# Performance work log

Measured on AMD Instinct MI355X. Metric: run time of the kernel, lower is better.

Reference implementation:

```python
import jax, jax.numpy as jnp
import numpy as np

B, S, D = 4, 1024, 1024
H = 16
DK = D // H  # 64
F = 4096
EPS = 1e-6


def layer_norm(x, gamma, beta):
    mu = jnp.mean(x, axis=-1, keepdims=True)
    var = jnp.mean(jnp.square(x - mu), axis=-1, keepdims=True)
    return (x - mu) * jax.lax.rsqrt(var + EPS) * gamma + beta


def setup_inputs() -> dict:
    key = jax.random.key(0)
    ks = jax.random.split(key, 16)
    sd = 0.02
    return {
        "x": jax.random.normal(ks[0], (B, S, D), dtype=jnp.float32),
        "Wq": jax.random.normal(ks[1], (H, D, DK), dtype=jnp.float32) * sd,
        "bq": jnp.zeros((H, DK), dtype=jnp.float32),
        "Wk": jax.random.normal(ks[2], (H, D, DK), dtype=jnp.float32) * sd,
        "bk": jnp.zeros((H, DK), dtype=jnp.float32),
        "Wv": jax.random.normal(ks[3], (H, D, DK), dtype=jnp.float32) * sd,
        "bv": jnp.zeros((H, DK), dtype=jnp.float32),
        "Wo": jax.random.normal(ks[4], (D, D), dtype=jnp.float32) * sd,
        "bo": jnp.zeros((D,), dtype=jnp.float32),
        "W1": jax.random.normal(ks[5], (D, F), dtype=jnp.float32) * sd,
        "b1": jnp.zeros((F,), dtype=jnp.float32),
        "W2": jax.random.normal(ks[6], (F, D), dtype=jnp.float32) * sd,
        "b2": jnp.zeros((D,), dtype=jnp.float32),
        "g1": jnp.ones((D,), dtype=jnp.float32),
        "be1": jnp.zeros((D,), dtype=jnp.float32),
        "g2": jnp.ones((D,), dtype=jnp.float32),
        "be2": jnp.zeros((D,), dtype=jnp.float32),
    }


def reference(x, Wq, bq, Wk, bk, Wv, bv, Wo, bo, W1, b1, W2, b2, g1, be1, g2, be2):
    # Per-head Dense projections, expressed as one batched einsum.
    # q/k/v: [B, H, S, DK]
    q = jnp.einsum('bsd,hdk->bhsk', x, Wq) + bq[:, None, :]
    k = jnp.einsum('bsd,hdk->bhsk', x, Wk) + bk[:, None, :]
    v = jnp.einsum('bsd,hdk->bhsk', x, Wv) + bv[:, None, :]
    scale = 1.0 / jnp.sqrt(jnp.float32(DK))
    scores = jnp.einsum('bhqk,bhsk->bhqs', q, k) * scale  # [B,H,S,S]
    attn = jax.nn.softmax(scores, axis=-1)
    ctx = jnp.einsum('bhqs,bhsk->bhqk', attn, v)  # [B,H,S,DK]
    # concat heads along last dim -> [B,S,D]
    ctx = jnp.transpose(ctx, (0, 2, 1, 3)).reshape(B, S, D)
    mh = ctx @ Wo + bo
    # dropout is identity at inference
    h1 = layer_norm(mh + x, g1, be1)
    ffn = jax.nn.relu(h1 @ W1 + b1) @ W2 + b2
    out = layer_norm(h1 + ffn, g2, be2)
    return out
```

## Files before the change

kernel.cpp:

```cpp
#include <hip/hip_runtime.h>
#include <hip/hip_bf16.h>
#include <stdint.h>


typedef __bf16 bf16x8 __attribute__((ext_vector_type(8)));
typedef float f32x4 __attribute__((ext_vector_type(4)));

__device__ __forceinline__ f32x4 mfma16(bf16x8 a, bf16x8 b, f32x4 c) {
  return __builtin_amdgcn_mfma_f32_16x16x32_bf16(a, b, c, 0, 0, 0);
}

__device__ __forceinline__ void gload_lds16(const void* g, void* l) {
  typedef const unsigned int __attribute__((address_space(1)))* GP;
  typedef unsigned int __attribute__((address_space(3)))* LP;
  __builtin_amdgcn_global_load_lds((GP)(uintptr_t)g,
                                   (LP)(unsigned int)(uintptr_t)l, 16, 0, 0);
}

template <int EPI>
__global__ __launch_bounds__(256, 2) void gemm_bt(
    const __bf16* __restrict__ A, const __bf16* __restrict__ BT,
    const float* __restrict__ bias, float* __restrict__ Cf,
    __bf16* __restrict__ Cb, int M, int N, int K)
{
  __shared__ __attribute__((aligned(16))) __bf16 As[128 * 32];
  __shared__ __attribute__((aligned(16))) __bf16 Bs[128 * 32];
  const int tid = threadIdx.x;
  const int lane = tid & 63;
  const int w = tid >> 6;
  const int wr = w >> 1, wc = w & 1;
  const int l15 = lane & 15, lhi = lane >> 4;
  const int m0 = blockIdx.y * 128, n0 = blockIdx.x * 128;

  const f32x4 fz = {0.f, 0.f, 0.f, 0.f};
  f32x4 acc[4][4];
#pragma unroll
  for (int i = 0; i < 4; i++)
#pragma unroll
    for (int j = 0; j < 4; j++) acc[i][j] = fz;

  const int arow = tid >> 2;
  const int acol = (tid & 3) * 8;
  const __bf16* Ag = A + (long)(m0 + arow) * K + acol;
  const __bf16* Bg = BT + (long)(n0 + arow) * K + acol;
  __bf16* Al = &As[tid * 8];
  __bf16* Bl = &Bs[tid * 8];

  for (int k0 = 0; k0 < K; k0 += 32) {
    gload_lds16(Ag + k0, Al);
    gload_lds16(Ag + k0 + 64 * (long)K, Al + 2048);
    gload_lds16(Bg + k0, Bl);
    gload_lds16(Bg + k0 + 64 * (long)K, Bl + 2048);
    __syncthreads();
    bf16x8 a[4], b[4];
#pragma unroll
    for (int i = 0; i < 4; i++) {
      a[i] = *(const bf16x8*)&As[(wr * 64 + i * 16 + l15) * 32 + lhi * 8];
      b[i] = *(const bf16x8*)&Bs[(wc * 64 + i * 16 + l15) * 32 + lhi * 8];
    }
#pragma unroll
    for (int i = 0; i < 4; i++)
#pragma unroll
      for (int j = 0; j < 4; j++) acc[i][j] = mfma16(a[i], b[j], acc[i][j]);
    __syncthreads();
  }

  if (EPI == 0) {
#pragma unroll
    for (int i = 0; i < 4; i++) {
      const int mB = m0 + wr * 64 + i * 16 + lhi * 4;
#pragma unroll
      for (int j = 0; j < 4; j++) {
        const int n = n0 + wc * 64 + j * 16 + l15;
        const float bs = bias[n];
#pragma unroll
        for (int r = 0; r < 4; r++)
          Cf[(long)(mB + r) * N + n] = acc[i][j][r] + bs;
      }
    }
  } else if (EPI == 1) {
#pragma unroll
    for (int i = 0; i < 4; i++) {
      const int mB = m0 + wr * 64 + i * 16 + lhi * 4;
#pragma unroll
      for (int j = 0; j < 4; j++) {
        const int n = n0 + wc * 64 + j * 16 + l15;
        const float bs = bias[n];
#pragma unroll
        for (int r = 0; r < 4; r++) {
          float v = acc[i][j][r] + bs;
          v = v > 0.f ? v : 0.f;
          Cb[(long)(mB + r) * N + n] = (__bf16)v;
        }
      }
    }
  } else {
#pragma unroll
    for (int i = 0; i < 4; i++) {
      const int mB = m0 + wr * 64 + i * 16 + lhi * 4;
#pragma unroll
      for (int j = 0; j < 4; j++) {
        const int n = n0 + wc * 64 + j * 16 + l15;
        const int proj = n >> 10, h = (n >> 6) & 15, dk = n & 63;
        const float bs = bias[n];
#pragma unroll
        for (int r = 0; r < 4; r++) {
          const int m = mB + r;
          const int b = m >> 10, sidx = m & 1023;
          Cb[(long)proj * 4194304 +
             ((long)(b * 16 + h) * 1024 + sidx) * 64 + dk] =
              (__bf16)(acc[i][j][r] + bs);
        }
      }
    }
  }
}

__global__ __launch_bounds__(256, 2) void attn_kernel(
    const __bf16* __restrict__ qg_, const __bf16* __restrict__ kg_,
    const __bf16* __restrict__ vg_, __bf16* __restrict__ ctx)
{
  __shared__ __attribute__((aligned(16))) __bf16 Ks[64 * 64];
  __shared__ __attribute__((aligned(16))) __bf16 Vt[64 * 64];
  __shared__ __attribute__((aligned(16))) __bf16 Ps[4][16 * 64];
  const int tid = threadIdx.x, lane = tid & 63, w = tid >> 6;
  const int l15 = lane & 15, lhi = lane >> 4;
  const int bh = blockIdx.y;
  const int b = bh >> 4, h = bh & 15;
  const int q0 = blockIdx.x * 64 + w * 16;

  const __bf16* qg = qg_ + ((long)bh * 1024 + q0) * 64;
  const __bf16* kg = kg_ + (long)bh * 1024 * 64;
  const __bf16* vg = vg_ + (long)bh * 1024 * 64;

  bf16x8 qa[2];
  qa[0] = *(const bf16x8*)&qg[l15 * 64 + lhi * 8];
  qa[1] = *(const bf16x8*)&qg[l15 * 64 + 32 + lhi * 8];

  const f32x4 fz = {0.f, 0.f, 0.f, 0.f};
  float mrun[4], lrun[4];
  f32x4 o[4];
#pragma unroll
  for (int r = 0; r < 4; r++) { mrun[r] = -1e30f; lrun[r] = 0.f; }
#pragma unroll
  for (int n = 0; n < 4; n++) o[n] = fz;

  const int lr = tid >> 2;
  const int lc = (tid & 3) * 16;

  for (int t = 0; t < 16; ++t) {
    __syncthreads();
    {
      const __bf16* krow = kg + (long)(t * 64 + lr) * 64 + lc;
      *(int4*)&Ks[lr * 64 + lc] = *(const int4*)krow;
      *(int4*)&Ks[lr * 64 + lc + 8] = *(const int4*)(krow + 8);
      const __bf16* vrow = vg + (long)(t * 64 + lr) * 64 + lc;
      int4 v0 = *(const int4*)vrow;
      int4 v1 = *(const int4*)(vrow + 8);
      const __bf16* e0 = (const __bf16*)&v0;
      const __bf16* e1 = (const __bf16*)&v1;
#pragma unroll
      for (int j = 0; j < 8; j++) Vt[(lc + j) * 64 + lr] = e0[j];
#pragma unroll
      for (int j = 0; j < 8; j++) Vt[(lc + 8 + j) * 64 + lr] = e1[j];
    }
    __syncthreads();

    f32x4 s[4];
#pragma unroll
    for (int n = 0; n < 4; n++) s[n] = fz;
#pragma unroll
    for (int kk = 0; kk < 2; kk++)
#pragma unroll
      for (int n = 0; n < 4; n++) {
        bf16x8 kb =
            *(const bf16x8*)&Ks[(n * 16 + l15) * 64 + kk * 32 + lhi * 8];
        s[n] = mfma16(qa[kk], kb, s[n]);
      }

    float alpha[4];
    float p[4][4];
#pragma unroll
    for (int r = 0; r < 4; r++) {
      float mx = -1e30f;
#pragma unroll
      for (int n = 0; n < 4; n++) {
        s[n][r] *= 0.125f;
        mx = fmaxf(mx, s[n][r]);
      }
#pragma unroll
      for (int off = 8; off; off >>= 1) mx = fmaxf(mx, __shfl_xor(mx, off));
      const float mnew = fmaxf(mrun[r], mx);
      alpha[r] = __expf(mrun[r] - mnew);
      float ps = 0.f;
#pragma unroll
      for (int n = 0; n < 4; n++) {
        const float pv = __expf(s[n][r] - mnew);
        p[n][r] = pv;
        ps += pv;
      }
#pragma unroll
      for (int off = 8; off; off >>= 1) ps += __shfl_xor(ps, off);
      mrun[r] = mnew;
      lrun[r] = lrun[r] * alpha[r] + ps;
    }
#pragma unroll
    for (int n = 0; n < 4; n++)
#pragma unroll
      for (int r = 0; r < 4; r++) o[n][r] *= alpha[r];

#pragma unroll
    for (int n = 0; n < 4; n++)
#pragma unroll
      for (int r = 0; r < 4; r++)
        Ps[w][(lhi * 4 + r) * 64 + n * 16 + l15] = (__bf16)p[n][r];
    asm volatile("s_waitcnt lgkmcnt(0)" ::: "memory");

#pragma unroll
    for (int kk = 0; kk < 2; kk++) {
      bf16x8 pa = *(const bf16x8*)&Ps[w][l15 * 64 + kk * 32 + lhi * 8];
#pragma unroll
      for (int n = 0; n < 4; n++) {
        bf16x8 vb =
            *(const bf16x8*)&Vt[(n * 16 + l15) * 64 + kk * 32 + lhi * 8];
        o[n] = mfma16(pa, vb, o[n]);
      }
    }
  }

  const long crow = (long)b * 1024 + q0;
#pragma unroll
  for (int n = 0; n < 4; n++)
#pragma unroll
    for (int r = 0; r < 4; r++) {
      const float val = o[n][r] / lrun[r];
      ctx[(crow + lhi * 4 + r) * 1024 + h * 64 + n * 16 + l15] = (__bf16)val;
    }
}

__global__ __launch_bounds__(256) void ln_kernel(
    const float* __restrict__ a, const float* __restrict__ b,
    const float* __restrict__ gamma, const float* __restrict__ beta,
    float* __restrict__ outf, __bf16* __restrict__ outb)
{
  const int row = blockIdx.x;
  const int tid = threadIdx.x;
  const float4 va = ((const float4*)(a + (long)row * 1024))[tid];
  const float4 vb = ((const float4*)(b + (long)row * 1024))[tid];
  const float x0 = va.x + vb.x, x1 = va.y + vb.y, x2 = va.z + vb.z,
              x3 = va.w + vb.w;
  float sum = x0 + x1 + x2 + x3;
  float sq = x0 * x0 + x1 * x1 + x2 * x2 + x3 * x3;
#pragma unroll
  for (int off = 32; off; off >>= 1) {
    sum += __shfl_down(sum, off);
    sq += __shfl_down(sq, off);
  }
  __shared__ float red[8];
  const int w = tid >> 6;
  if ((tid & 63) == 0) { red[w] = sum; red[4 + w] = sq; }
  __syncthreads();
  sum = red[0] + red[1] + red[2] + red[3];
  sq = red[4] + red[5] + red[6] + red[7];
  const float mean = sum * (1.f / 1024.f);
  const float var = sq * (1.f / 1024.f) - mean * mean;
  const float inv = rsqrtf(var + 1e-6f);
  const float4 g = ((const float4*)gamma)[tid];
  const float4 be = ((const float4*)beta)[tid];
  const float y0 = (x0 - mean) * inv * g.x + be.x;
  const float y1 = (x1 - mean) * inv * g.y + be.y;
  const float y2 = (x2 - mean) * inv * g.z + be.z;
  const float y3 = (x3 - mean) * inv * g.w + be.w;
  float4 o4; o4.x = y0; o4.y = y1; o4.z = y2; o4.w = y3;
  ((float4*)(outf + (long)row * 1024))[tid] = o4;
  if (outb) {
    __bf16* ob = outb + (long)row * 1024 + tid * 4;
    ob[0] = (__bf16)y0; ob[1] = (__bf16)y1;
    ob[2] = (__bf16)y2; ob[3] = (__bf16)y3;
  }
}

__global__ __launch_bounds__(256) void cast_bf16_kernel(
    const float* __restrict__ in, __bf16* __restrict__ out, int n4)
{
  const int i = blockIdx.x * 256 + threadIdx.x;
  if (i < n4) {
    const float4 v = ((const float4*)in)[i];
    __bf16* o = out + (long)i * 4;
    o[0] = (__bf16)v.x; o[1] = (__bf16)v.y;
    o[2] = (__bf16)v.z; o[3] = (__bf16)v.w;
  }
}

__global__ __launch_bounds__(256) void pack_bias_kernel(
    const float* __restrict__ bq, const float* __restrict__ bk,
    const float* __restrict__ bv, float* __restrict__ out)
{
  const int i = blockIdx.x * 256 + threadIdx.x;
  if (i < 3072) {
    const float* src = i < 1024 ? bq : (i < 2048 ? bk : bv);
    out[i] = src[i & 1023];
  }
}

__global__ __launch_bounds__(256) void transpose_cast_kernel(
    const float* __restrict__ in, __bf16* __restrict__ out, int R, int C,
    long ibs, long obs)
{
  __shared__ float t[32][33];
  const float* ip = in + (long)blockIdx.z * ibs;
  __bf16* op = out + (long)blockIdx.z * obs;
  const int c0 = blockIdx.x * 32, r0 = blockIdx.y * 32;
  const int tx = threadIdx.x & 31, ty = threadIdx.x >> 5;
#pragma unroll
  for (int i = 0; i < 32; i += 8)
    t[ty + i][tx] = ip[(long)(r0 + ty + i) * C + (c0 + tx)];
  __syncthreads();
#pragma unroll
  for (int i = 0; i < 32; i += 8)
    op[(long)(c0 + ty + i) * R + (r0 + tx)] = (__bf16)t[tx][ty + i];
}

extern "C" void kernel_launch(void* const* d_in, const int* in_sizes, int n_in,
                              void* d_out, int out_size, void* d_ws,
                              size_t ws_size, hipStream_t stream)
{
  const float* x   = (const float*)d_in[0];
  const float* Wq  = (const float*)d_in[1];
  const float* bq  = (const float*)d_in[2];
  const float* Wk  = (const float*)d_in[3];
  const float* bk  = (const float*)d_in[4];
  const float* Wv  = (const float*)d_in[5];
  const float* bv  = (const float*)d_in[6];
  const float* Wo  = (const float*)d_in[7];
  const float* bo  = (const float*)d_in[8];
  const float* W1  = (const float*)d_in[9];
  const float* b1  = (const float*)d_in[10];
  const float* W2  = (const float*)d_in[11];
  const float* b2  = (const float*)d_in[12];
  const float* g1  = (const float*)d_in[13];
  const float* be1 = (const float*)d_in[14];
  const float* g2  = (const float*)d_in[15];
  const float* be2 = (const float*)d_in[16];
  float* out = (float*)d_out;

  char* ws = (char*)d_ws;
  __bf16* wqkvT = (__bf16*)(ws);
  __bf16* woT   = (__bf16*)(ws + 6291456);
  __bf16* w1T   = (__bf16*)(ws + 8388608);
  __bf16* w2T   = (__bf16*)(ws + 16777216);
  float*  bqkv  = (float*)(ws + 25165824);
  __bf16* xbf   = (__bf16*)(ws + 25178112);
  __bf16* ctxb  = xbf;
  __bf16* qkv   = (__bf16*)(ws + 33566720);
  __bf16* h1b   = (__bf16*)(ws + 33566720);
  __bf16* f1b   = (__bf16*)(ws + 41955328);
  float*  h1    = (float*)(ws + 75509760);
  float*  mh    = out;
  float*  f2    = out;

  cast_bf16_kernel<<<4096, 256, 0, stream>>>(x, xbf, 1048576);
  pack_bias_kernel<<<12, 256, 0, stream>>>(bq, bk, bv, bqkv);
  transpose_cast_kernel<<<dim3(2, 32, 16), 256, 0, stream>>>(
      Wq, wqkvT, 1024, 64, 65536, 65536);
  transpose_cast_kernel<<<dim3(2, 32, 16), 256, 0, stream>>>(
      Wk, wqkvT + 1048576, 1024, 64, 65536, 65536);
  transpose_cast_kernel<<<dim3(2, 32, 16), 256, 0, stream>>>(
      Wv, wqkvT + 2097152, 1024, 64, 65536, 65536);
  transpose_cast_kernel<<<dim3(32, 32, 1), 256, 0, stream>>>(
      Wo, woT, 1024, 1024, 0, 0);
  transpose_cast_kernel<<<dim3(128, 32, 1), 256, 0, stream>>>(
      W1, w1T, 1024, 4096, 0, 0);
  transpose_cast_kernel<<<dim3(32, 128, 1), 256, 0, stream>>>(
      W2, w2T, 4096, 1024, 0, 0);

  gemm_bt<2><<<dim3(24, 32), 256, 0, stream>>>(
      xbf, wqkvT, bqkv, nullptr, qkv, 4096, 3072, 1024);

  attn_kernel<<<dim3(16, 64), 256, 0, stream>>>(
      qkv, qkv + 4194304, qkv + 8388608, ctxb);

  gemm_bt<0><<<dim3(8, 32), 256, 0, stream>>>(
      ctxb, woT, bo, mh, nullptr, 4096, 1024, 1024);

  ln_kernel<<<4096, 256, 0, stream>>>(mh, x, g1, be1, h1, h1b);

  gemm_bt<1><<<dim3(32, 32), 256, 0, stream>>>(
      h1b, w1T, b1, nullptr, f1b, 4096, 4096, 1024);
  gemm_bt<0><<<dim3(8, 32), 256, 0, stream>>>(
      f1b, w2T, b2, f2, nullptr, 4096, 1024, 4096);

  ln_kernel<<<4096, 256, 0, stream>>>(f2, h1, g2, be2, out, nullptr);
}
```

Before: 438.7 us.

## Double-buffer attention K/V tiles with async LDS loads and pre-transposed V

Adds a separate kernel that transposes V into a per-head [DK,S] layout in the output buffer. The attention kernel then streams K and the transposed V tiles into double-buffered shared memory with direct global-to-LDS loads, overlapping the next tile's load with the current tile's compute. XOR swizzling removes LDS bank conflicts, and s_setprio boosts the MFMA sections. It costs an extra launch and a round trip of V through memory, but removes the scalar in-loop transpose and one barrier per tile.

```diff
diff --git a/kernel.cpp b/kernel.cpp
--- a/kernel.cpp
+++ b/kernel.cpp
@@ -116,12 +116,28 @@
   }
 }
 
+__global__ __launch_bounds__(256) void vtrans_kernel(
+    const __bf16* __restrict__ in, __bf16* __restrict__ out)
+{
+  __shared__ __bf16 t[64][66];
+  const int bh = blockIdx.y, s0 = blockIdx.x * 64;
+  const int tx = threadIdx.x & 63, ty = threadIdx.x >> 6;
+  const __bf16* ip = in + (long)bh * 65536 + (long)s0 * 64;
+  __bf16* op = out + (long)bh * 65536;
+#pragma unroll
+  for (int i = 0; i < 64; i += 4) t[ty + i][tx] = ip[(ty + i) * 64 + tx];
+  __syncthreads();
+#pragma unroll
+  for (int i = 0; i < 64; i += 4)
+    op[(long)(ty + i) * 1024 + s0 + tx] = t[tx][ty + i];
+}
+
 __global__ __launch_bounds__(256, 2) void attn_kernel(
     const __bf16* __restrict__ qg_, const __bf16* __restrict__ kg_,
-    const __bf16* __restrict__ vg_, __bf16* __restrict__ ctx)
-{
-  __shared__ __attribute__((aligned(16))) __bf16 Ks[64 * 64];
-  __shared__ __attribute__((aligned(16))) __bf16 Vt[64 * 64];
+    const __bf16* __restrict__ vtg_, __bf16* __restrict__ ctx)
+{
+  __shared__ __attribute__((aligned(16))) __bf16 Kb[2][64 * 64];
+  __shared__ __attribute__((aligned(16))) __bf16 Vb[2][64 * 64];
   __shared__ __attribute__((aligned(16))) __bf16 Ps[4][16 * 64];
   const int tid = threadIdx.x, lane = tid & 63, w = tid >> 6;
   const int l15 = lane & 15, lhi = lane >> 4;
@@ -130,13 +146,22 @@
   const int q0 = blockIdx.x * 64 + w * 16;
 
   const __bf16* qg = qg_ + ((long)bh * 1024 + q0) * 64;
-  const __bf16* kg = kg_ + (long)bh * 1024 * 64;
-  const __bf16* vg = vg_ + (long)bh * 1024 * 64;
+  const __bf16* kg = kg_ + (long)bh * 65536;
+  const __bf16* vtg = vtg_ + (long)bh * 65536;
 
   bf16x8 qa[2];
   qa[0] = *(const bf16x8*)&qg[l15 * 64 + lhi * 8];
   qa[1] = *(const bf16x8*)&qg[l15 * 64 + 32 + lhi * 8];
 
+  const int srow0 = tid >> 3;
+  const int srow1 = srow0 + 32;
+  const int sw0 = (tid & 7) ^ (srow0 & 7);
+  const int sw1 = (tid & 7) ^ (srow1 & 7);
+  const __bf16* kst0 = kg + srow0 * 64 + sw0 * 8;
+  const __bf16* kst1 = kg + srow1 * 64 + sw1 * 8;
+  const __bf16* vst0 = vtg + srow0 * 1024 + sw0 * 8;
+  const __bf16* vst1 = vtg + srow1 * 1024 + sw1 * 8;
+
   const f32x4 fz = {0.f, 0.f, 0.f, 0.f};
   float mrun[4], lrun[4];
   f32x4 o[4];
@@ -145,38 +170,44 @@
 #pragma unroll
   for (int n = 0; n < 4; n++) o[n] = fz;
 
-  const int lr = tid >> 2;
-  const int lc = (tid & 3) * 16;
-
+  const int e = l15 & 7;
+  const int c0 = (lhi ^ e) * 8;
+  const int c1 = ((4 | lhi) ^ e) * 8;
+
+  {
+    __bf16* kb = &Kb[0][tid * 8];
+    __bf16* vb = &Vb[0][tid * 8];
+    gload_lds16(kst0, kb);
+    gload_lds16(kst1, kb + 2048);
+    gload_lds16(vst0, vb);
+    gload_lds16(vst1, vb + 2048);
+  }
+
+  int cur = 0;
   for (int t = 0; t < 16; ++t) {
     __syncthreads();
-    {
-      const __bf16* krow = kg + (long)(t * 64 + lr) * 64 + lc;
-      *(int4*)&Ks[lr * 64 + lc] = *(const int4*)krow;
-      *(int4*)&Ks[lr * 64 + lc + 8] = *(const int4*)(krow + 8);
-      const __bf16* vrow = vg + (long)(t * 64 + lr) * 64 + lc;
-      int4 v0 = *(const int4*)vrow;
-      int4 v1 = *(const int4*)(vrow + 8);
-      const __bf16* e0 = (const __bf16*)&v0;
-      const __bf16* e1 = (const __bf16*)&v1;
-#pragma unroll
-      for (int j = 0; j < 8; j++) Vt[(lc + j) * 64 + lr] = e0[j];
-#pragma unroll
-      for (int j = 0; j < 8; j++) Vt[(lc + 8 + j) * 64 + lr] = e1[j];
-    }
-    __syncthreads();
+    if (t + 1 < 16) {
+      __bf16* kb = &Kb[cur ^ 1][tid * 8];
+      __bf16* vb = &Vb[cur ^ 1][tid * 8];
+      gload_lds16(kst0 + (t + 1) * 4096, kb);
+      gload_lds16(kst1 + (t + 1) * 4096, kb + 2048);
+      gload_lds16(vst0 + (t + 1) * 64, vb);
+      gload_lds16(vst1 + (t + 1) * 64, vb + 2048);
+    }
 
     f32x4 s[4];
 #pragma unroll
     for (int n = 0; n < 4; n++) s[n] = fz;
-#pragma unroll
-    for (int kk = 0; kk < 2; kk++)
-#pragma unroll
-      for (int n = 0; n < 4; n++) {
-        bf16x8 kb =
-            *(const bf16x8*)&Ks[(n * 16 + l15) * 64 + kk * 32 + lhi * 8];
-        s[n] = mfma16(qa[kk], kb, s[n]);
-      }
+    __builtin_amdgcn_s_setprio(1);
+#pragma unroll
+    for (int n = 0; n < 4; n++) {
+      const int row = (n * 16 + l15) * 64;
+      bf16x8 kb0 = *(const bf16x8*)&Kb[cur][row + c0];
+      bf16x8 kb1 = *(const bf16x8*)&Kb[cur][row + c1];
+      s[n] = mfma16(qa[0], kb0, s[n]);
+      s[n] = mfma16(qa[1], kb1, s[n]);
+    }
+    __builtin_amdgcn_s_setprio(0);
 
     float alpha[4];
     float p[4][4];
@@ -210,22 +241,28 @@
       for (int r = 0; r < 4; r++) o[n][r] *= alpha[r];
 
 #pragma unroll
-    for (int n = 0; n < 4; n++)
-#pragma unroll
-      for (int r = 0; r < 4; r++)
-        Ps[w][(lhi * 4 + r) * 64 + n * 16 + l15] = (__bf16)p[n][r];
+    for (int n = 0; n < 4; n++) {
+      const int ch = n * 2 + (l15 >> 3);
+#pragma unroll
+      for (int r = 0; r < 4; r++) {
+        const int row = lhi * 4 + r;
+        Ps[w][row * 64 + (ch ^ (row & 7)) * 8 + e] = (__bf16)p[n][r];
+      }
+    }
     asm volatile("s_waitcnt lgkmcnt(0)" ::: "memory");
 
+    __builtin_amdgcn_s_setprio(1);
 #pragma unroll
     for (int kk = 0; kk < 2; kk++) {
-      bf16x8 pa = *(const bf16x8*)&Ps[w][l15 * 64 + kk * 32 + lhi * 8];
+      bf16x8 pa = *(const bf16x8*)&Ps[w][l15 * 64 + (kk ? c1 : c0)];
 #pragma unroll
       for (int n = 0; n < 4; n++) {
-        bf16x8 vb =
-            *(const bf16x8*)&Vt[(n * 16 + l15) * 64 + kk * 32 + lhi * 8];
+        bf16x8 vb = *(const bf16x8*)&Vb[cur][(n * 16 + l15) * 64 + (kk ? c1 : c0)];
         o[n] = mfma16(pa, vb, o[n]);
       }
     }
+    __builtin_amdgcn_s_setprio(0);
+    cur ^= 1;
   }
 
   const long crow = (long)b * 1024 + q0;
@@ -356,6 +393,7 @@
   __bf16* h1b   = (__bf16*)(ws + 33566720);
   __bf16* f1b   = (__bf16*)(ws + 41955328);
   float*  h1    = (float*)(ws + 75509760);
+  __bf16* vt    = (__bf16*)d_out;
   float*  mh    = out;
   float*  f2    = out;
 
@@ -377,8 +415,10 @@
   gemm_bt<2><<<dim3(24, 32), 256, 0, stream>>>(
       xbf, wqkvT, bqkv, nullptr, qkv, 4096, 3072, 1024);
 
+  vtrans_kernel<<<dim3(16, 64), 256, 0, stream>>>(qkv + 8388608, vt);
+
   attn_kernel<<<dim3(16, 64), 256, 0, stream>>>(
-      qkv, qkv + 4194304, qkv + 8388608, ctxb);
+      qkv, qkv + 4194304, vt, ctxb);
 
   gemm_bt<0><<<dim3(8, 32), 256, 0, stream>>>(
       ctxb, woT, bo, mh, nullptr, 4096, 1024, 1024);
```

After: 412.2 us. -6.0%, faster.
